# Performance work log

Measured on AMD Instinct MI355X. Metric: run time of the kernel, lower is better.

The kernel has to match this reference:

```python
import jax, jax.numpy as jnp
import numpy as np

N = 100_000      # nodes
E = 1_600_000    # edges (avg degree 16)
F_IN = 128       # num_features
HID = 64         # width
C = 40           # num_classes


def setup_inputs() -> dict:
    key = jax.random.key(0)
    ks = jax.random.split(key, 8)
    x = jax.random.normal(ks[0], (N, F_IN), jnp.float32)
    edge_index = jax.random.randint(ks[1], (2, E), 0, N, dtype=jnp.int32)
    # Xavier-uniform-like scaled weights (matches nn.init.xavier_uniform_ statistics)
    def xavier(k, fan_in, fan_out):
        lim = np.sqrt(6.0 / (fan_in + fan_out)).astype(np.float32)
        return jax.random.uniform(k, (fan_in, fan_out), jnp.float32, -lim, lim)
    return {
        "x": x,
        "edge_index": edge_index,
        "W1": xavier(ks[2], F_IN, HID), "b1": jnp.zeros((HID,), jnp.float32),
        "W2": xavier(ks[3], HID, HID),  "b2": jnp.zeros((HID,), jnp.float32),
        "W3": xavier(ks[4], HID, C),    "b3": jnp.zeros((C,), jnp.float32),
    }


def _gcn_forward(x, edge_index, W1, b1, W2, b2, W3, b3):
    n = x.shape[0]
    loops = jnp.arange(n, dtype=edge_index.dtype)
    src = jnp.concatenate([edge_index[0], loops])  # row (source)
    dst = jnp.concatenate([edge_index[1], loops])  # col (target)
    # symmetric GCN normalization with self-loops (PyG gcn_norm, edge_weight=1)
    deg = jax.ops.segment_sum(jnp.ones_like(dst, x.dtype), dst, num_segments=n)
    dis = jnp.where(deg > 0, jax.lax.rsqrt(jnp.maximum(deg, 1e-12)), 0.0)
    norm = (dis[src] * dis[dst])[:, None]  # [E+N, 1]

    def conv(h, W, b):
        h = h @ W                                                   # [n, out]
        agg = jax.ops.segment_sum(h[src] * norm, dst, num_segments=n)
        return agg + b

    h = conv(x, W1, b1)
    h = h * jax.nn.sigmoid(h)   # swish
    h = conv(h, W2, b2)
    h = h * jax.nn.sigmoid(h)   # swish
    return jax.nn.log_softmax(conv(h, W3, b3), axis=1)


def reference(x, edge_index, W1, b1, W2, b2, W3, b3):
    return _gcn_forward(x, edge_index, W1, b1, W2, b2, W3, b3)
```

## Files before the change

### kernel.cpp

```cpp
#include <hip/hip_runtime.h>
#include <math.h>

#define THREADS 256
#define S1THREADS 512
#define BSHIFT 9
#define BSIZE (1 << BSHIFT)
#define PASS1_CHUNK 4096
#define SRC_BITS 17
#define S2CAP 12288

typedef unsigned int u32;
typedef unsigned short u16;
typedef __attribute__((ext_vector_type(8))) short short8v;
typedef __attribute__((ext_vector_type(4))) float float4v;

__device__ __forceinline__ u16 f2bf(float f) {
    u32 u = __float_as_uint(f);
    u = (u + 0x7fffu + ((u >> 16) & 1u)) >> 16;
    return (u16)u;
}
__device__ __forceinline__ float bf_lo(u32 u) { return __uint_as_float(u << 16); }
__device__ __forceinline__ float bf_hi(u32 u) { return __uint_as_float(u & 0xffff0000u); }


__global__ __launch_bounds__(S1THREADS) void hist_kernel(
    const int* __restrict__ dst, int* __restrict__ hmat, int e, int nbuck)
{
    __shared__ int hist[BSIZE];
    const int tid = threadIdx.x;
    const int c0  = blockIdx.x * PASS1_CHUNK;
    for (int i = tid; i < nbuck; i += S1THREADS) hist[i] = 0;
    __syncthreads();
    for (int i = tid; i < PASS1_CHUNK; i += S1THREADS) {
        int idx = c0 + i;
        if (idx < e) atomicAdd(&hist[dst[idx] >> BSHIFT], 1);
    }
    __syncthreads();
    for (int b = tid; b < nbuck; b += S1THREADS)
        hmat[blockIdx.x * nbuck + b] = hist[b];
}


__global__ __launch_bounds__(THREADS) void colscan_kernel(
    const int* __restrict__ hmat, int* __restrict__ bmat,
    int* __restrict__ bcnt, int nblk, int nbuck)
{
    __shared__ int s[THREADS];
    const int b = blockIdx.x, tid = threadIdx.x;
    int run = 0;
    for (int t0 = 0; t0 < nblk; t0 += THREADS) {
        int idx = t0 + tid;
        int v = (idx < nblk) ? hmat[idx * nbuck + b] : 0;
        s[tid] = v;
        __syncthreads();
        for (int off = 1; off < THREADS; off <<= 1) {
            int t = (tid >= off) ? s[tid - off] : 0;
            __syncthreads();
            s[tid] += t;
            __syncthreads();
        }
        if (idx < nblk) bmat[idx * nbuck + b] = run + s[tid] - v;
        run += s[THREADS - 1];
        __syncthreads();
    }
    if (tid == 0) bcnt[b] = run;
}


__global__ __launch_bounds__(1024) void bscan_kernel(const int* __restrict__ bcnt,
                                                     int* __restrict__ bbase,
                                                     int* __restrict__ rowptr,
                                                     int nbuck, int n, int e) {
    __shared__ int s[1024];
    int v = (threadIdx.x < nbuck) ? bcnt[threadIdx.x] : 0;
    s[threadIdx.x] = v;
    __syncthreads();
    for (int off = 1; off < 1024; off <<= 1) {
        int t = (threadIdx.x >= off) ? s[threadIdx.x - off] : 0;
        __syncthreads();
        s[threadIdx.x] += t;
        __syncthreads();
    }
    if (threadIdx.x < nbuck) bbase[threadIdx.x] = s[threadIdx.x] - v;
    if (threadIdx.x == 0) rowptr[n] = e;
}


__global__ __launch_bounds__(S1THREADS) void scatter_kernel(
    const int* __restrict__ src, const int* __restrict__ dst,
    const int* __restrict__ bmat, const int* __restrict__ bbase,
    u32* __restrict__ pairs, int e, int nbuck)
{
    __shared__ int base_s[BSIZE], cur[BSIZE];
    const int tid = threadIdx.x;
    const int c0  = blockIdx.x * PASS1_CHUNK;
    for (int b = tid; b < nbuck; b += S1THREADS) {
        base_s[b] = bbase[b] + bmat[blockIdx.x * nbuck + b];
        cur[b] = 0;
    }
    __syncthreads();
    for (int i = tid; i < PASS1_CHUNK; i += S1THREADS) {
        int idx = c0 + i;
        if (idx < e) {
            int d = dst[idx];
            int b = d >> BSHIFT;
            int off = atomicAdd(&cur[b], 1);
            pairs[base_s[b] + off] = ((u32)(d & (BSIZE - 1)) << SRC_BITS) | (u32)src[idx];
        }
    }
}


__global__ __launch_bounds__(S1THREADS) void sort2_kernel(
    const int* __restrict__ bbase, const u32* __restrict__ pairs,
    int* __restrict__ rowptr, float* __restrict__ dis,
    int* __restrict__ csr, int n, int e)
{
    __shared__ int cnt[BSIZE];
    __shared__ int cur[BSIZE];
    __shared__ int s2[S1THREADS];
    __shared__ u32 pst[S2CAP];

    const int b  = blockIdx.x;
    const int d0 = b << BSHIFT;
    const int nd = min(BSIZE, n - d0);
    const int p0 = bbase[b];
    const int p1 = (d0 + nd >= n) ? e : bbase[b + 1];
    const int sz = p1 - p0;
    const int tid = threadIdx.x;

    for (int i = tid; i < BSIZE; i += S1THREADS) cnt[i] = 0;
    __syncthreads();

    for (int j = tid; j < sz; j += S1THREADS) {
        u32 pr = pairs[p0 + j];
        if (j < S2CAP) pst[j] = pr;
        atomicAdd(&cnt[pr >> SRC_BITS], 1);
    }
    __syncthreads();

    int v = cnt[tid];
    s2[tid] = v;
    __syncthreads();
    for (int off = 1; off < S1THREADS; off <<= 1) {
        int t = (tid >= off) ? s2[tid - off] : 0;
        __syncthreads();
        s2[tid] += t;
        __syncthreads();
    }
    cur[tid] = p0 + s2[tid] - v;
    __syncthreads();

    for (int i = tid; i < nd; i += S1THREADS) {
        rowptr[d0 + i] = cur[i];
        dis[d0 + i] = rsqrtf((float)(cnt[i] + 1));
    }
    __syncthreads();

    for (int j = tid; j < sz; j += S1THREADS) {
        u32 pr = (j < S2CAP) ? pst[j] : pairs[p0 + j];
        int pos = atomicAdd(&cur[pr >> SRC_BITS], 1);
        csr[pos] = (int)(pr & ((1u << SRC_BITS) - 1));
    }
}

template <int KTOT, int OUT, int SOUT, bool PRE>
__global__ __launch_bounds__(THREADS) void mfma_gemm_kernel(
    const float* __restrict__ Xf, const u16* __restrict__ Xb,
    const float* __restrict__ W, const float* __restrict__ bin,
    const float* __restrict__ dis, u16* __restrict__ hs, int n)
{
    constexpr int NCG = (OUT + 15) / 16;
    constexpr int CC  = NCG * 16;
    constexpr int NKK = KTOT / 32;
    constexpr int WS  = KTOT + 8;

    __shared__ u16 WT[CC][WS];

    const int tid = threadIdx.x;

    for (int idx = tid; idx < KTOT * CC; idx += THREADS) {
        int k = idx / CC;
        int c = idx - k * CC;
        float v = (c < OUT) ? W[k * OUT + c] : 0.f;
        WT[c][k] = f2bf(v);
    }
    __syncthreads();

    const int lane  = tid & 63;
    const int rlane = lane & 15;
    const int kgrp  = lane >> 4;
    const int rbase = blockIdx.x * 64 + (tid >> 6) * 16;

    const int arow = min(rbase + rlane, n - 1);

    float4v acc[NCG];
#pragma unroll
    for (int g = 0; g < NCG; ++g) acc[g] = (float4v)(0.f);

    float dd_a = PRE ? dis[arow] : 0.f;

#pragma unroll
    for (int kk = 0; kk < NKK; ++kk) {
        const int kb = kk * 32 + kgrp * 8;
        short8v a;
        if (PRE) {
            uint4 u = *(const uint4*)(Xb + (size_t)arow * KTOT + kb);
            u32 w[4] = {u.x, u.y, u.z, u.w};
#pragma unroll
            for (int q = 0; q < 4; ++q) {
                float h0 = bf_lo(w[q]) * dd_a + bin[kb + 2 * q];
                float h1 = bf_hi(w[q]) * dd_a + bin[kb + 2 * q + 1];
                a[2 * q]     = (short)f2bf(h0 / (1.f + __expf(-h0)));
                a[2 * q + 1] = (short)f2bf(h1 / (1.f + __expf(-h1)));
            }
        } else {
            float4 f0 = *(const float4*)(Xf + (size_t)arow * KTOT + kb);
            float4 f1 = *(const float4*)(Xf + (size_t)arow * KTOT + kb + 4);
            a[0] = (short)f2bf(f0.x); a[1] = (short)f2bf(f0.y);
            a[2] = (short)f2bf(f0.z); a[3] = (short)f2bf(f0.w);
            a[4] = (short)f2bf(f1.x); a[5] = (short)f2bf(f1.y);
            a[6] = (short)f2bf(f1.z); a[7] = (short)f2bf(f1.w);
        }
#pragma unroll
        for (int g = 0; g < NCG; ++g) {
            short8v b = *(const short8v*)&WT[g * 16 + rlane][kb];
            acc[g] = __builtin_amdgcn_mfma_f32_16x16x32_bf16(a, b, acc[g], 0, 0, 0);
        }
    }

#pragma unroll
    for (int j = 0; j < 4; ++j) {
        int row = rbase + kgrp * 4 + j;
        if (row < n) {
            float dd = dis[row];
#pragma unroll
            for (int g = 0; g < NCG; ++g) {
                int col = g * 16 + rlane;
                if (OUT == CC || col < OUT)
                    hs[(size_t)row * SOUT + col] = f2bf(acc[g][j] * dd);
            }
        }
    }
}

__global__ __launch_bounds__(THREADS) void agg64_kernel(
    const int* __restrict__ rowptr, const int* __restrict__ csr,
    const u16* __restrict__ hs, u16* __restrict__ agg, int n)
{
    const int lane = threadIdx.x & 63;
    const int sub  = lane >> 3;
    const int gl   = lane & 7;
    const int d = (blockIdx.x * 4 + (threadIdx.x >> 6)) * 8 + sub;
    if (d >= n) return;
    const int c8 = gl * 8;

    const int beg = rowptr[d], end = rowptr[d + 1];
    float acc[8];
    {
        uint4 u = *(const uint4*)(hs + (size_t)d * 64 + c8);
        acc[0] = bf_lo(u.x); acc[1] = bf_hi(u.x);
        acc[2] = bf_lo(u.y); acc[3] = bf_hi(u.y);
        acc[4] = bf_lo(u.z); acc[5] = bf_hi(u.z);
        acc[6] = bf_lo(u.w); acc[7] = bf_hi(u.w);
    }

    int eidx = (beg + gl < end) ? csr[beg + gl] : 0;
    for (int t = beg; t < end; t += 8) {
        const int m = end - t;
        uint4 ub[8];
#pragma unroll
        for (int q = 0; q < 8; ++q) {
            int s = __shfl(eidx, (sub << 3) + q);
            if (q < m) ub[q] = *(const uint4*)(hs + (size_t)s * 64 + c8);
        }
        int eidx_n = (t + 8 + gl < end) ? csr[t + 8 + gl] : 0;
#pragma unroll
        for (int q = 0; q < 8; ++q) {
            if (q < m) {
                acc[0] += bf_lo(ub[q].x); acc[1] += bf_hi(ub[q].x);
                acc[2] += bf_lo(ub[q].y); acc[3] += bf_hi(ub[q].y);
                acc[4] += bf_lo(ub[q].z); acc[5] += bf_hi(ub[q].z);
                acc[6] += bf_lo(ub[q].w); acc[7] += bf_hi(ub[q].w);
            }
        }
        eidx = eidx_n;
    }

    uint4 o;
    o.x = (u32)f2bf(acc[0]) | ((u32)f2bf(acc[1]) << 16);
    o.y = (u32)f2bf(acc[2]) | ((u32)f2bf(acc[3]) << 16);
    o.z = (u32)f2bf(acc[4]) | ((u32)f2bf(acc[5]) << 16);
    o.w = (u32)f2bf(acc[6]) | ((u32)f2bf(acc[7]) << 16);
    *(uint4*)(agg + (size_t)d * 64 + c8) = o;
}

__global__ __launch_bounds__(THREADS) void agg40_lsm_kernel(
    const int* __restrict__ rowptr, const int* __restrict__ csr,
    const u16* __restrict__ hs, const float* __restrict__ dis,
    const float* __restrict__ b3, float* __restrict__ out, int n)
{
    constexpr int S = 48;
    const int lane = threadIdx.x & 63;
    const int sub  = lane >> 3;
    const int gl   = lane & 7;
    const int d = (blockIdx.x * 4 + (threadIdx.x >> 6)) * 8 + sub;
    if (d >= n) return;
    const bool act = (gl < 5);
    const int c8 = gl * 8;

    const int beg = rowptr[d], end = rowptr[d + 1];
    float acc[8] = {0.f,0.f,0.f,0.f,0.f,0.f,0.f,0.f};
    if (act) {
        uint4 u = *(const uint4*)(hs + (size_t)d * S + c8);
        acc[0] = bf_lo(u.x); acc[1] = bf_hi(u.x);
        acc[2] = bf_lo(u.y); acc[3] = bf_hi(u.y);
        acc[4] = bf_lo(u.z); acc[5] = bf_hi(u.z);
        acc[6] = bf_lo(u.w); acc[7] = bf_hi(u.w);
    }

    int eidx = (beg + gl < end) ? csr[beg + gl] : 0;
    for (int t = beg; t < end; t += 8) {
        const int m = end - t;
        uint4 ub[8];
#pragma unroll
        for (int q = 0; q < 8; ++q) {
            int s = __shfl(eidx, (sub << 3) + q);
            if (q < m && act) ub[q] = *(const uint4*)(hs + (size_t)s * S + c8);
        }
        int eidx_n = (t + 8 + gl < end) ? csr[t + 8 + gl] : 0;
#pragma unroll
        for (int q = 0; q < 8; ++q) {
            if (q < m && act) {
                acc[0] += bf_lo(ub[q].x); acc[1] += bf_hi(ub[q].x);
                acc[2] += bf_lo(ub[q].y); acc[3] += bf_hi(ub[q].y);
                acc[4] += bf_lo(ub[q].z); acc[5] += bf_hi(ub[q].z);
                acc[6] += bf_lo(ub[q].w); acc[7] += bf_hi(ub[q].w);
            }
        }
        eidx = eidx_n;
    }

    float val[8];
    float mx = -1e30f;
    if (act) {
        float dd = dis[d];
#pragma unroll
        for (int q = 0; q < 8; ++q) {
            val[q] = acc[q] * dd + b3[c8 + q];
            mx = fmaxf(mx, val[q]);
        }
    }
#pragma unroll
    for (int off = 4; off > 0; off >>= 1) mx = fmaxf(mx, __shfl_xor(mx, off));
    float es = 0.f;
    if (act) {
#pragma unroll
        for (int q = 0; q < 8; ++q) es += __expf(val[q] - mx);
    }
#pragma unroll
    for (int off = 4; off > 0; off >>= 1) es += __shfl_xor(es, off);
    float lse = mx + __logf(es);
    if (act) {
        float4 o0 = make_float4(val[0]-lse, val[1]-lse, val[2]-lse, val[3]-lse);
        float4 o1 = make_float4(val[4]-lse, val[5]-lse, val[6]-lse, val[7]-lse);
        *(float4*)(out + (size_t)d * 40 + c8)     = o0;
        *(float4*)(out + (size_t)d * 40 + c8 + 4) = o1;
    }
}

static inline size_t align_up(size_t v, size_t a) { return (v + a - 1) & ~(a - 1); }

extern "C" void kernel_launch(void* const* d_in, const int* in_sizes, int n_in,
                              void* d_out, int out_size, void* d_ws, size_t ws_size,
                              hipStream_t stream) {
    const float* x  = (const float*)d_in[0];
    const int*   ei = (const int*)d_in[1];
    const float* W1 = (const float*)d_in[2];
    const float* b1 = (const float*)d_in[3];
    const float* W2 = (const float*)d_in[4];
    const float* b2 = (const float*)d_in[5];
    const float* W3 = (const float*)d_in[6];
    const float* b3 = (const float*)d_in[7];
    float* out = (float*)d_out;

    const int n = in_sizes[0] / 128;
    const int e = in_sizes[1] / 2;
    const int* src = ei;
    const int* dst = ei + e;

    const int nbuck = (n + BSIZE - 1) >> BSHIFT;
    const int nblk  = (e + PASS1_CHUNK - 1) / PASS1_CHUNK;

    char* base = (char*)d_ws;
    size_t off = 0;
    float* dis = (float*)(base + off);    off = align_up(off + (size_t)n * 4, 256);
    int* rowptr = (int*)(base + off);     off = align_up(off + (size_t)(n + 1) * 4, 256);
    int* bcnt = (int*)(base + off);       off = align_up(off + 1024 * 4, 256);
    int* bbase = (int*)(base + off);      off = align_up(off + 1025 * 4, 256);
    int* hmat = (int*)(base + off);       off = align_up(off + (size_t)nblk * nbuck * 4, 256);
    int* bmat = (int*)(base + off);       off = align_up(off + (size_t)nblk * nbuck * 4, 256);
    int* csr = (int*)(base + off);        off = align_up(off + (size_t)e * 4, 256);
    u16* hsb = (u16*)(base + off);        off = align_up(off + (size_t)n * 64 * 2, 256);
    u16* aggb = (u16*)(base + off);       off = align_up(off + (size_t)n * 64 * 2, 256);
    u32* pairs = (u32*)hsb;

    const int gb_rows = (n + 63) / 64;
    const int gb_agg  = (n + 31) / 32;

    hist_kernel<<<nblk, S1THREADS, 0, stream>>>(dst, hmat, e, nbuck);
    colscan_kernel<<<nbuck, THREADS, 0, stream>>>(hmat, bmat, bcnt, nblk, nbuck);
    bscan_kernel<<<1, 1024, 0, stream>>>(bcnt, bbase, rowptr, nbuck, n, e);
    scatter_kernel<<<nblk, S1THREADS, 0, stream>>>(src, dst, bmat, bbase, pairs, e, nbuck);
    sort2_kernel<<<nbuck, S1THREADS, 0, stream>>>(bbase, pairs, rowptr, dis, csr, n, e);

    mfma_gemm_kernel<128, 64, 64, false><<<gb_rows, THREADS, 0, stream>>>(
        x, nullptr, W1, nullptr, dis, hsb, n);
    agg64_kernel<<<gb_agg, THREADS, 0, stream>>>(rowptr, csr, hsb, aggb, n);

    mfma_gemm_kernel<64, 64, 64, true><<<gb_rows, THREADS, 0, stream>>>(
        nullptr, aggb, W2, b1, dis, hsb, n);
    agg64_kernel<<<gb_agg, THREADS, 0, stream>>>(rowptr, csr, hsb, aggb, n);

    mfma_gemm_kernel<64, 40, 48, true><<<gb_rows, THREADS, 0, stream>>>(
        nullptr, aggb, W3, b2, dis, hsb, n);
    agg40_lsm_kernel<<<gb_agg, THREADS, 0, stream>>>(rowptr, csr, hsb, dis, b3, out, n);
}
```

Baseline: 181.5 us.

## Fuse neighbor aggregation with the following layer's GEMM via shared memory

Each 64-row block now runs the 64-wide neighbor aggregation, applies the norm scale, bias and swish, stages the bf16 result in LDS, and then runs the next layer's MFMA GEMM from LDS. This removes the separate aggregate buffer's global write and read and two kernel launches. Output ping-pongs between two hs buffers so the gather never reads rows being overwritten. The cost is more LDS per block and 64 rows per block instead of 32, which changes occupancy and load balance in the gather phase.

```diff
diff --git a/kernel.cpp b/kernel.cpp
--- a/kernel.cpp
+++ b/kernel.cpp
@@ -164,10 +164,9 @@
     }
 }
 
-template <int KTOT, int OUT, int SOUT, bool PRE>
+template <int KTOT, int OUT, int SOUT>
 __global__ __launch_bounds__(THREADS) void mfma_gemm_kernel(
-    const float* __restrict__ Xf, const u16* __restrict__ Xb,
-    const float* __restrict__ W, const float* __restrict__ bin,
+    const float* __restrict__ Xf, const float* __restrict__ W,
     const float* __restrict__ dis, u16* __restrict__ hs, int n)
 {
     constexpr int NCG = (OUT + 15) / 16;
@@ -178,7 +177,6 @@
     __shared__ u16 WT[CC][WS];
 
     const int tid = threadIdx.x;
-
     for (int idx = tid; idx < KTOT * CC; idx += THREADS) {
         int k = idx / CC;
         int c = idx - k * CC;
@@ -191,37 +189,22 @@
     const int rlane = lane & 15;
     const int kgrp  = lane >> 4;
     const int rbase = blockIdx.x * 64 + (tid >> 6) * 16;
-
     const int arow = min(rbase + rlane, n - 1);
 
     float4v acc[NCG];
 #pragma unroll
     for (int g = 0; g < NCG; ++g) acc[g] = (float4v)(0.f);
-
-    float dd_a = PRE ? dis[arow] : 0.f;
 
 #pragma unroll
     for (int kk = 0; kk < NKK; ++kk) {
         const int kb = kk * 32 + kgrp * 8;
         short8v a;
-        if (PRE) {
-            uint4 u = *(const uint4*)(Xb + (size_t)arow * KTOT + kb);
-            u32 w[4] = {u.x, u.y, u.z, u.w};
-#pragma unroll
-            for (int q = 0; q < 4; ++q) {
-                float h0 = bf_lo(w[q]) * dd_a + bin[kb + 2 * q];
-                float h1 = bf_hi(w[q]) * dd_a + bin[kb + 2 * q + 1];
-                a[2 * q]     = (short)f2bf(h0 / (1.f + __expf(-h0)));
-                a[2 * q + 1] = (short)f2bf(h1 / (1.f + __expf(-h1)));
-            }
-        } else {
-            float4 f0 = *(const float4*)(Xf + (size_t)arow * KTOT + kb);
-            float4 f1 = *(const float4*)(Xf + (size_t)arow * KTOT + kb + 4);
-            a[0] = (short)f2bf(f0.x); a[1] = (short)f2bf(f0.y);
-            a[2] = (short)f2bf(f0.z); a[3] = (short)f2bf(f0.w);
-            a[4] = (short)f2bf(f1.x); a[5] = (short)f2bf(f1.y);
-            a[6] = (short)f2bf(f1.z); a[7] = (short)f2bf(f1.w);
-        }
+        float4 f0 = *(const float4*)(Xf + (size_t)arow * KTOT + kb);
+        float4 f1 = *(const float4*)(Xf + (size_t)arow * KTOT + kb + 4);
+        a[0] = (short)f2bf(f0.x); a[1] = (short)f2bf(f0.y);
+        a[2] = (short)f2bf(f0.z); a[3] = (short)f2bf(f0.w);
+        a[4] = (short)f2bf(f1.x); a[5] = (short)f2bf(f1.y);
+        a[6] = (short)f2bf(f1.z); a[7] = (short)f2bf(f1.w);
 #pragma unroll
         for (int g = 0; g < NCG; ++g) {
             short8v b = *(const short8v*)&WT[g * 16 + rlane][kb];
@@ -244,55 +227,118 @@
     }
 }
 
-__global__ __launch_bounds__(THREADS) void agg64_kernel(
+template <int OUT, int SOUT>
+__global__ __launch_bounds__(THREADS) void fused_agg_gemm_kernel(
     const int* __restrict__ rowptr, const int* __restrict__ csr,
-    const u16* __restrict__ hs, u16* __restrict__ agg, int n)
-{
-    const int lane = threadIdx.x & 63;
+    const u16* __restrict__ hs, const float* __restrict__ W,
+    const float* __restrict__ bin, const float* __restrict__ dis,
+    u16* __restrict__ hsout, int n)
+{
+    constexpr int KTOT = 64;
+    constexpr int NCG = (OUT + 15) / 16;
+    constexpr int CC  = NCG * 16;
+    constexpr int WS  = KTOT + 8;
+
+    __shared__ u16 WT[CC][WS];
+    __shared__ u16 As[64][WS];
+
+    const int tid = threadIdx.x;
+    for (int idx = tid; idx < KTOT * CC; idx += THREADS) {
+        int k = idx / CC;
+        int c = idx - k * CC;
+        float v = (c < OUT) ? W[k * OUT + c] : 0.f;
+        WT[c][k] = f2bf(v);
+    }
+
+    const int lane = tid & 63;
+    const int wid  = tid >> 6;
     const int sub  = lane >> 3;
     const int gl   = lane & 7;
-    const int d = (blockIdx.x * 4 + (threadIdx.x >> 6)) * 8 + sub;
-    if (d >= n) return;
-    const int c8 = gl * 8;
-
-    const int beg = rowptr[d], end = rowptr[d + 1];
-    float acc[8];
-    {
-        uint4 u = *(const uint4*)(hs + (size_t)d * 64 + c8);
-        acc[0] = bf_lo(u.x); acc[1] = bf_hi(u.x);
-        acc[2] = bf_lo(u.y); acc[3] = bf_hi(u.y);
-        acc[4] = bf_lo(u.z); acc[5] = bf_hi(u.z);
-        acc[6] = bf_lo(u.w); acc[7] = bf_hi(u.w);
-    }
-
-    int eidx = (beg + gl < end) ? csr[beg + gl] : 0;
-    for (int t = beg; t < end; t += 8) {
-        const int m = end - t;
-        uint4 ub[8];
-#pragma unroll
-        for (int q = 0; q < 8; ++q) {
-            int s = __shfl(eidx, (sub << 3) + q);
-            if (q < m) ub[q] = *(const uint4*)(hs + (size_t)s * 64 + c8);
-        }
-        int eidx_n = (t + 8 + gl < end) ? csr[t + 8 + gl] : 0;
-#pragma unroll
-        for (int q = 0; q < 8; ++q) {
-            if (q < m) {
-                acc[0] += bf_lo(ub[q].x); acc[1] += bf_hi(ub[q].x);
-                acc[2] += bf_lo(ub[q].y); acc[3] += bf_hi(ub[q].y);
-                acc[4] += bf_lo(ub[q].z); acc[5] += bf_hi(ub[q].z);
-                acc[6] += bf_lo(ub[q].w); acc[7] += bf_hi(ub[q].w);
-            }
-        }
-        eidx = eidx_n;
-    }
-
-    uint4 o;
-    o.x = (u32)f2bf(acc[0]) | ((u32)f2bf(acc[1]) << 16);
-    o.y = (u32)f2bf(acc[2]) | ((u32)f2bf(acc[3]) << 16);
-    o.z = (u32)f2bf(acc[4]) | ((u32)f2bf(acc[5]) << 16);
-    o.w = (u32)f2bf(acc[6]) | ((u32)f2bf(acc[7]) << 16);
-    *(uint4*)(agg + (size_t)d * 64 + c8) = o;
+    const int c8   = gl * 8;
+    const int row0 = blockIdx.x * 64;
+
+#pragma unroll
+    for (int half = 0; half < 2; ++half) {
+        const int lr = half * 32 + wid * 8 + sub;
+        const int d  = row0 + lr;
+        if (d < n) {
+            const int beg = rowptr[d], end = rowptr[d + 1];
+            float acc[8];
+            {
+                uint4 u = *(const uint4*)(hs + (size_t)d * 64 + c8);
+                acc[0] = bf_lo(u.x); acc[1] = bf_hi(u.x);
+                acc[2] = bf_lo(u.y); acc[3] = bf_hi(u.y);
+                acc[4] = bf_lo(u.z); acc[5] = bf_hi(u.z);
+                acc[6] = bf_lo(u.w); acc[7] = bf_hi(u.w);
+            }
+            int eidx = (beg + gl < end) ? csr[beg + gl] : 0;
+            for (int t = beg; t < end; t += 8) {
+                const int m = end - t;
+                uint4 ub[8];
+#pragma unroll
+                for (int q = 0; q < 8; ++q) {
+                    int s = __shfl(eidx, (sub << 3) + q);
+                    if (q < m) ub[q] = *(const uint4*)(hs + (size_t)s * 64 + c8);
+                }
+                int eidx_n = (t + 8 + gl < end) ? csr[t + 8 + gl] : 0;
+#pragma unroll
+                for (int q = 0; q < 8; ++q) {
+                    if (q < m) {
+                        acc[0] += bf_lo(ub[q].x); acc[1] += bf_hi(ub[q].x);
+                        acc[2] += bf_lo(ub[q].y); acc[3] += bf_hi(ub[q].y);
+                        acc[4] += bf_lo(ub[q].z); acc[5] += bf_hi(ub[q].z);
+                        acc[6] += bf_lo(ub[q].w); acc[7] += bf_hi(ub[q].w);
+                    }
+                }
+                eidx = eidx_n;
+            }
+            float dd = dis[d];
+            u16 o[8];
+#pragma unroll
+            for (int q = 0; q < 8; ++q) {
+                float h = acc[q] * dd + bin[c8 + q];
+                o[q] = f2bf(h / (1.f + __expf(-h)));
+            }
+            ushort4 o0 = {o[0], o[1], o[2], o[3]};
+            ushort4 o1 = {o[4], o[5], o[6], o[7]};
+            *(ushort4*)&As[lr][c8]     = o0;
+            *(ushort4*)&As[lr][c8 + 4] = o1;
+        }
+    }
+    __syncthreads();
+
+    const int rlane = lane & 15;
+    const int kgrp  = lane >> 4;
+    const int rbase = row0 + wid * 16;
+
+    float4v acc[NCG];
+#pragma unroll
+    for (int g = 0; g < NCG; ++g) acc[g] = (float4v)(0.f);
+
+#pragma unroll
+    for (int kk = 0; kk < 2; ++kk) {
+        const int kb = kk * 32 + kgrp * 8;
+        short8v a = *(const short8v*)&As[wid * 16 + rlane][kb];
+#pragma unroll
+        for (int g = 0; g < NCG; ++g) {
+            short8v b = *(const short8v*)&WT[g * 16 + rlane][kb];
+            acc[g] = __builtin_amdgcn_mfma_f32_16x16x32_bf16(a, b, acc[g], 0, 0, 0);
+        }
+    }
+
+#pragma unroll
+    for (int j = 0; j < 4; ++j) {
+        int row = rbase + kgrp * 4 + j;
+        if (row < n) {
+            float dd = dis[row];
+#pragma unroll
+            for (int g = 0; g < NCG; ++g) {
+                int col = g * 16 + rlane;
+                if (OUT == CC || col < OUT)
+                    hsout[(size_t)row * SOUT + col] = f2bf(acc[g][j] * dd);
+            }
+        }
+    }
 }
 
 __global__ __launch_bounds__(THREADS) void agg40_lsm_kernel(
@@ -402,7 +448,7 @@
     int* bmat = (int*)(base + off);       off = align_up(off + (size_t)nblk * nbuck * 4, 256);
     int* csr = (int*)(base + off);        off = align_up(off + (size_t)e * 4, 256);
     u16* hsb = (u16*)(base + off);        off = align_up(off + (size_t)n * 64 * 2, 256);
-    u16* aggb = (u16*)(base + off);       off = align_up(off + (size_t)n * 64 * 2, 256);
+    u16* hs2b = (u16*)(base + off);       off = align_up(off + (size_t)n * 64 * 2, 256);
     u32* pairs = (u32*)hsb;
 
     const int gb_rows = (n + 63) / 64;
@@ -414,15 +460,13 @@
     scatter_kernel<<<nblk, S1THREADS, 0, stream>>>(src, dst, bmat, bbase, pairs, e, nbuck);
     sort2_kernel<<<nbuck, S1THREADS, 0, stream>>>(bbase, pairs, rowptr, dis, csr, n, e);
 
-    mfma_gemm_kernel<128, 64, 64, false><<<gb_rows, THREADS, 0, stream>>>(
-        x, nullptr, W1, nullptr, dis, hsb, n);
-    agg64_kernel<<<gb_agg, THREADS, 0, stream>>>(rowptr, csr, hsb, aggb, n);
-
-    mfma_gemm_kernel<64, 64, 64, true><<<gb_rows, THREADS, 0, stream>>>(
-        nullptr, aggb, W2, b1, dis, hsb, n);
-    agg64_kernel<<<gb_agg, THREADS, 0, stream>>>(rowptr, csr, hsb, aggb, n);
-
-    mfma_gemm_kernel<64, 40, 48, true><<<gb_rows, THREADS, 0, stream>>>(
-        nullptr, aggb, W3, b2, dis, hsb, n);
+    mfma_gemm_kernel<128, 64, 64><<<gb_rows, THREADS, 0, stream>>>(x, W1, dis, hsb, n);
+
+    fused_agg_gemm_kernel<64, 64><<<gb_rows, THREADS, 0, stream>>>(
+        rowptr, csr, hsb, W2, b1, dis, hs2b, n);
+
+    fused_agg_gemm_kernel<40, 48><<<gb_rows, THREADS, 0, stream>>>(
+        rowptr, csr, hs2b, W3, b2, dis, hsb, n);
+
     agg40_lsm_kernel<<<gb_agg, THREADS, 0, stream>>>(rowptr, csr, hsb, dis, b3, out, n);
 }
```

After: 176.0 us. -3.1%, faster.
